# Kernel optimization log

Hardware: AMD Instinct MI355X
Metric: run time of the kernel (lower is better)

Reference implementation:

```python
import jax, jax.numpy as jnp
import numpy as np

N = 128
MAX_LEN = 1024
L = 1024
BATCH = 32


def _legs_transition(n):
    # HiPPO-LegS A, B matrices (float64 numpy, matches torch module's transition())
    q = np.arange(n, dtype=np.float64)
    col, row = np.meshgrid(q, q)
    r = 2 * q + 1
    M = -(np.where(row >= col, r, 0) - np.diag(q))
    T = np.sqrt(np.diag(2 * q + 1))
    A = T @ M @ np.linalg.inv(T)
    B = np.diag(T)
    return A, B


def _stacked_bilinear(n, max_length):
    # Bilinear discretization per timestep t: (I - A/(2t))^{-1} (I + A/(2t)), (I - A/(2t))^{-1} B/t
    A, B = _legs_transition(n)
    t = np.arange(1, max_length + 1, dtype=np.float64)[:, None, None]  # (L,1,1)
    I = np.eye(n)
    At = A[None] / t                                   # (L,N,N)
    lhs = I - At / 2
    A_st = np.linalg.solve(lhs, I + At / 2)            # (L,N,N)
    Bt = (B[None, :] / t[:, 0, 0][:, None])[..., None]  # (L,N,1)
    B_st = np.linalg.solve(lhs, Bt)[..., 0]            # (L,N)
    return A_st.astype(np.float32), B_st.astype(np.float32)


def setup_inputs() -> dict:
    key = jax.random.key(0)
    inputs = jax.random.normal(key, (L, BATCH), dtype=jnp.float32)
    A_st, B_st = _stacked_bilinear(N, MAX_LEN)
    return {
        "inputs": inputs,
        "A_stacked": jnp.asarray(A_st),
        "B_stacked": jnp.asarray(B_st),
    }


def reference(inputs, A_stacked, B_stacked):
    # inputs: (L, B); A_stacked: (L, N, N); B_stacked: (L, N)
    Lc = inputs.shape[0]
    u = inputs[..., None] * B_stacked[:Lc, None, :]  # (L, B, N)

    def step(s, Au):
        A_t, u_t = Au                                 # (N,N), (B,N)
        s = jnp.einsum("ij,bj->bi", A_t, s) + u_t
        return s, s

    s0 = jnp.zeros_like(u[0])
    _, xs = jax.lax.scan(step, s0, (A_stacked[:Lc], u))
    return xs  # (L, B, N)
```

## Files before the change

kernel.cpp:

```cpp
#include <hip/hip_runtime.h>


#define LDK 136
#define PKF 11264

using f16 = _Float16;
typedef __attribute__((ext_vector_type(8))) f16 f16x8;
typedef __attribute__((ext_vector_type(4))) f16 f16x4;
typedef __attribute__((ext_vector_type(4))) float f32x4;

__device__ __forceinline__ f32x4 mfma3(f16x8 ah, f16x8 al, f16x8 bh, f16x8 bl,
                                       f32x4 c) {
  c = __builtin_amdgcn_mfma_f32_16x16x32_f16(ah, bh, c, 0, 0, 0);
  c = __builtin_amdgcn_mfma_f32_16x16x32_f16(ah, bl, c, 0, 0, 0);
  c = __builtin_amdgcn_mfma_f32_16x16x32_f16(al, bh, c, 0, 0, 0);
  return c;
}

__device__ __forceinline__ void split8(const float* v, f16x8& h, f16x8& l) {
#pragma unroll
  for (int j = 0; j < 8; ++j) {
    const float x = v[j];
    const f16 hh = (f16)x;
    h[j] = hh;
    l[j] = (f16)(x - (float)hh);
  }
}

__device__ __forceinline__ int slot2mt(int h, int slot) {
  if (h == 0) return (slot & 1) ? 7 - (slot >> 1) : (slot >> 1);
  return (slot & 1) ? 5 - (slot >> 1) : 2 + (slot >> 1);
}

__device__ __forceinline__ void gload_lds16(const float* g, float* l) {
  __builtin_amdgcn_global_load_lds(
      (const __attribute__((address_space(1))) unsigned int*)g,
      (__attribute__((address_space(3))) unsigned int*)l, 16, 0, 0);
}

__device__ __forceinline__ void bar_nodrain() {
  __builtin_amdgcn_sched_barrier(0);
  asm volatile("s_waitcnt lgkmcnt(0)" ::: "memory");
  __builtin_amdgcn_s_barrier();
  __builtin_amdgcn_sched_barrier(0);
}
__device__ __forceinline__ void wait_vm0() {
  __builtin_amdgcn_sched_barrier(0);
  asm volatile("s_waitcnt vmcnt(0)" ::: "memory");
  __builtin_amdgcn_sched_barrier(0);
}

__device__ __forceinline__ int pk_src_off(int m) {
  int b, local, ccm1, sh;
  if (m < 128)      { b = 0; local = m;       ccm1 = 3;  sh = 2; }
  else if (m < 384) { b = 1; local = m - 128; ccm1 = 7;  sh = 3; }
  else if (m < 896) { b = 2; local = m - 384; ccm1 = 15; sh = 4; }
  else              { b = 3; local = m - 896; ccm1 = 15; sh = 4; }
  const int ri = local >> sh, cp = local & ccm1;
  const int c = cp ^ (ri & ccm1);
  return (b * 32 + ri) * 128 + c * 8;
}

__device__ __forceinline__ void read_pk(const f16* __restrict__ Bs, int nt,
                                        int lr, int j0, f16x8& v) {
  const int b = nt >> 1;
  const int ri = ((nt & 1) << 4) + lr;
  const int ccm1 = (b == 0) ? 3 : (b == 1) ? 7 : 15;
  const int fb = (b == 0) ? 0 : (b == 1) ? 1024 : (b == 2) ? 3072 : 7168;
  const int c = j0 ^ (ri & ccm1);
  v = *(const f16x8*)(Bs + fb + ri * ((ccm1 + 1) * 8) + c * 8);
}

template <int NT, int IT>
__device__ __forceinline__ void pk_precompute(int tid, int (&src)[IT]) {
#pragma unroll
  for (int it = 0; it < IT; ++it) {
    const int m = tid + it * NT;
    src[it] = (m < 1408) ? pk_src_off(m) : 0;
  }
}

template <int NT, int IT>
__device__ __forceinline__ void pk_stage(const f16* __restrict__ gMh,
                                         const f16* __restrict__ gMl,
                                         f16* __restrict__ dH,
                                         f16* __restrict__ dL,
                                         const int (&src)[IT], int tid) {
#pragma unroll
  for (int it = 0; it < IT; ++it) {
    const int m = tid + it * NT;
    if (m < 1408) {
      gload_lds16((const float*)(gMh + src[it]), (float*)(dH + m * 8));
      gload_lds16((const float*)(gMl + src[it]), (float*)(dL + m * 8));
    }
  }
}

__device__ __forceinline__ void compute_soff(int tid, int (&soff)[8]) {
#pragma unroll
  for (int it = 0; it < 8; ++it) {
    const int m = tid + it * 320;
    if (m < 2304) {
      const int kt = (m >= 768) + (m >= 1536) + (m >= 2048);
      const int local = m - ((kt >= 1) * 768 + (kt >= 2) * 768 + (kt >= 3) * 512);
      const int rp = local >> 3, c = local & 7;
      const int r = rp + 32 + (kt >= 2) * 32 + (kt >= 3) * 32;
      soff[it] = r * 128 + kt * 32 + ((c ^ (rp & 7)) << 2);
    } else {
      soff[it] = 0;
    }
  }
}

__device__ __forceinline__ void issue_A(const float* __restrict__ Al,
                                        float* __restrict__ Ast,
                                        const int (&soff)[8], int tid) {
#pragma unroll
  for (int it = 0; it < 8; ++it) {
    if (it < 7 || tid < 64)
      gload_lds16(Al + soff[it], Ast + (tid + it * 320) * 4);
  }
}

__device__ __forceinline__ void read_staged(const float* __restrict__ Ast,
                                            int nt, int kt, int lr, int q,
                                            f16x8& ch, f16x8& cl) {
  const int rp = nt * 16 + lr - (32 + (kt >= 2) * 32 + (kt >= 3) * 32);
  const float* pb =
      Ast + ((kt >= 1) * 3072 + (kt >= 2) * 3072 + (kt >= 3) * 2048) + rp * 32;
  float raw[8];
  *(float4*)&raw[0] = *(const float4*)(pb + (((2 * q + 0) ^ (rp & 7)) << 2));
  *(float4*)&raw[4] = *(const float4*)(pb + (((2 * q + 1) ^ (rp & 7)) << 2));
  split8(raw, ch, cl);
}

__device__ __forceinline__ void chain_step_k1a(const float* __restrict__ Acur,
                                               const float* __restrict__ Anext,
                                               const float* __restrict__ x32,
                                               const float* __restrict__ Bvl,
                                               f16* __restrict__ Ph,
                                               f16* __restrict__ Pl,
                                               const float* __restrict__ AstCur,
                                               float* __restrict__ AstNxt,
                                               const int (&soff)[8],
                                               int wv, int mt) {
  const int tid = threadIdx.x;
  const int lane = tid & 63, lr = lane & 15, q = lane >> 4;
  const bool wrow = (mt >= 8);
  const int ktA0 = wrow ? 0 : (mt >> 1);
  f16x8 ah[4], al[4];
#pragma unroll
  for (int kt = 0; kt < 4; ++kt) {
    if (kt >= ktA0) {
      const int off = (wv * 16 + lr) * LDK + kt * 32 + q * 8;
      ah[kt] = *(const f16x8*)(Ph + off);
      al[kt] = *(const f16x8*)(Pl + off);
    }
  }
  const bool need0 = wrow || mt == 0;
  const bool need1 = wrow || mt <= 1;
  float dir0[8], dir1[8];
  if (need0) {
    const float* p = Acur + lr * 128 + q * 8;
    *(float4*)&dir0[0] = *(const float4*)p;
    *(float4*)&dir0[4] = *(const float4*)(p + 4);
  }
  if (need1) {
    const float* p = Acur + (16 + lr) * 128 + q * 8;
    *(float4*)&dir1[0] = *(const float4*)p;
    *(float4*)&dir1[4] = *(const float4*)(p + 4);
  }
  float4 x4v = {0.f, 0.f, 0.f, 0.f};
  float bnv[8];
  if (wrow) {
    const int b0 = (mt - 8) * 16 + q * 4;
    x4v = *(const float4*)(x32 + b0);
#pragma unroll
    for (int nt = 0; nt < 8; ++nt) bnv[nt] = Bvl[nt * 16 + lr];
  }
  wait_vm0();
  bar_nodrain();
  if (Anext) issue_A(Anext, AstNxt, soff, tid);
  f32x4 acc[8];
#pragma unroll
  for (int nt = 0; nt < 8; ++nt) acc[nt] = (f32x4){0.f, 0.f, 0.f, 0.f};
#pragma unroll
  for (int nt = 2; nt < 8; ++nt) {
    if (wrow || nt >= mt) {
#pragma unroll
      for (int kt = 0; kt < 4; ++kt) {
        if (kt >= ktA0 && kt <= (nt >> 1)) {
          f16x8 ch, cl;
          read_staged(AstCur, nt, kt, lr, q, ch, cl);
          acc[nt] = mfma3(ah[kt], al[kt], ch, cl, acc[nt]);
        }
      }
    }
  }
  if (need0) {
    f16x8 ch, cl;
    split8(dir0, ch, cl);
    acc[0] = mfma3(ah[0], al[0], ch, cl, acc[0]);
  }
  if (need1) {
    f16x8 ch, cl;
    split8(dir1, ch, cl);
    acc[1] = mfma3(ah[0], al[0], ch, cl, acc[1]);
  }
#pragma unroll
  for (int nt = 0; nt < 8; ++nt) {
    if (!(wrow || nt >= mt)) continue;
    float v[4] = {acc[nt][0], acc[nt][1], acc[nt][2], acc[nt][3]};
    if (wrow) {
      v[0] += bnv[nt] * x4v.x; v[1] += bnv[nt] * x4v.y;
      v[2] += bnv[nt] * x4v.z; v[3] += bnv[nt] * x4v.w;
    }
#pragma unroll
    for (int r = 0; r < 4; ++r) {
      const int o = (wv * 16 + q * 4 + r) * LDK + nt * 16 + lr;
      const f16 hh = (f16)v[r];
      Ph[o] = hh;
      Pl[o] = (f16)(v[r] - (float)hh);
    }
  }
  bar_nodrain();
}

__device__ __forceinline__ void chain_copyout(const f16* __restrict__ Ph,
                                              const f16* __restrict__ Pl, int h,
                                              f16* __restrict__ oMh,
                                              f16* __restrict__ oMl,
                                              float* __restrict__ oW) {
  const int tid = threadIdx.x;
  for (int t = tid; t < 1024; t += 320) {
    const int i = t >> 3;
    const int slot = (t >> 1) & 3;
    const int half = t & 1;
    const int mtg = slot2mt(h, slot);
    const int y0 = mtg * 16 + half * 8;
    if ((y0 >> 5) > (i >> 5)) continue;
    f16x8 hv, lv;
#pragma unroll
    for (int e = 0; e < 8; ++e) {
      hv[e] = Ph[(slot * 16 + half * 8 + e) * LDK + i];
      lv[e] = Pl[(slot * 16 + half * 8 + e) * LDK + i];
    }
    *(f16x8*)(oMh + i * 128 + y0) = hv;
    *(f16x8*)(oMl + i * 128 + y0) = lv;
  }
  for (int t = tid; t < 512; t += 320) {
    const int n = t >> 2, b4 = (t & 3) * 4;
    float4 o;
    float* po = (float*)&o;
#pragma unroll
    for (int e = 0; e < 4; ++e)
      po[e] = (float)Ph[(64 + b4 + e) * LDK + n] + (float)Pl[(64 + b4 + e) * LDK + n];
    *(float4*)(oW + n * 32 + h * 16 + b4) = o;
  }
}

__device__ __forceinline__ void state_step_h_b16(const f16* __restrict__ Bh16,
                                                 const f16* __restrict__ Bl16,
                                                 const float* __restrict__ aux0,
                                                 f16* __restrict__ Sh,
                                                 f16* __restrict__ Sl, int h) {
  const int tid = threadIdx.x;
  const int wv4 = tid >> 6;
  const bool act = (wv4 < 4);
  const int wv = wv4 & 3;
  const int lane = tid & 63, lr = lane & 15, q = lane >> 4;
  const int nts[2] = {wv, 7 - wv};
  const int ktAmax = (7 - wv) >> 1;
  f16x8 ah[4], al[4];
  f16x8 bh[2][4], bl[2][4];
  f32x4 acc[2];
  if (act) {
#pragma unroll
    for (int kt = 0; kt < 4; ++kt)
      if (kt <= ktAmax) {
        const int off = lr * LDK + kt * 32 + q * 8;
        ah[kt] = *(const f16x8*)(Sh + off);
        al[kt] = *(const f16x8*)(Sl + off);
      }
#pragma unroll
    for (int ni = 0; ni < 2; ++ni) {
      const int nt = nts[ni];
#pragma unroll
      for (int kt = 0; kt < 4; ++kt)
        if (kt <= (nt >> 1)) {
          const int o = (nt * 16 + lr) * 128 + kt * 32 + q * 8;
          bh[ni][kt] = *(const f16x8*)(Bh16 + o);
          bl[ni][kt] = *(const f16x8*)(Bl16 + o);
        }
    }
#pragma unroll
    for (int ni = 0; ni < 2; ++ni) acc[ni] = (f32x4){0.f, 0.f, 0.f, 0.f};
#pragma unroll
    for (int ni = 0; ni < 2; ++ni) {
      const int nt = nts[ni];
#pragma unroll
      for (int kt = 0; kt < 4; ++kt)
        if (kt <= (nt >> 1))
          acc[ni] = mfma3(ah[kt], al[kt], bh[ni][kt], bl[ni][kt], acc[ni]);
    }
  }
  __syncthreads();
  if (act) {
#pragma unroll
    for (int ni = 0; ni < 2; ++ni) {
      const int nt = nts[ni];
      float v[4] = {acc[ni][0], acc[ni][1], acc[ni][2], acc[ni][3]};
      const int bq = q * 4;
      const float4 w4 = *(const float4*)(aux0 + (nt * 16 + lr) * 32 + h * 16 + bq);
      v[0] += w4.x; v[1] += w4.y; v[2] += w4.z; v[3] += w4.w;
#pragma unroll
      for (int r = 0; r < 4; ++r) {
        const int o = (bq + r) * LDK + nt * 16 + lr;
        const f16 hh = (f16)v[r];
        Sh[o] = hh;
        Sl[o] = (f16)(v[r] - (float)hh);
      }
    }
  }
  __syncthreads();
}

__device__ __forceinline__ void state_step_h_stagedA(
    const float* __restrict__ Acur, const float* __restrict__ Anext,
    const float* __restrict__ x32, const float* __restrict__ Bvl,
    f16* __restrict__ Sh, f16* __restrict__ Sl, float* __restrict__ outp,
    int h, const float* __restrict__ AstCur, float* __restrict__ AstNxt,
    const int (&soff)[8]) {
  const int tid = threadIdx.x;
  const int wv4 = tid >> 6;
  const bool act = (wv4 < 4);
  const int wv = wv4 & 3;
  const int lane = tid & 63, lr = lane & 15, q = lane >> 4;
  const int ntL = wv, ntH = 7 - wv;
  f16x8 ah[4], al[4];
  float dir[8];
  float4 x4v = {0.f, 0.f, 0.f, 0.f};
  float bnL = 0.f, bnH = 0.f;
  if (act) {
    const int ktAmax = ntH >> 1;
#pragma unroll
    for (int kt = 0; kt < 4; ++kt)
      if (kt <= ktAmax) {
        const int off = lr * LDK + kt * 32 + q * 8;
        ah[kt] = *(const f16x8*)(Sh + off);
        al[kt] = *(const f16x8*)(Sl + off);
      }
    if (wv < 2) {
      const float* p = Acur + (ntL * 16 + lr) * 128 + q * 8;
      *(float4*)&dir[0] = *(const float4*)p;
      *(float4*)&dir[4] = *(const float4*)(p + 4);
    }
    x4v = *(const float4*)(x32 + h * 16 + q * 4);
    bnL = Bvl[ntL * 16 + lr];
    bnH = Bvl[ntH * 16 + lr];
  }
  wait_vm0();
  bar_nodrain();
  if (Anext) issue_A(Anext, AstNxt, soff, tid);
  f32x4 accL = (f32x4){0.f, 0.f, 0.f, 0.f}, accH = accL;
  if (act) {
#pragma unroll
    for (int kt = 0; kt < 4; ++kt) {
      if (kt <= (ntH >> 1)) {
        f16x8 ch, cl;
        read_staged(AstCur, ntH, kt, lr, q, ch, cl);
        accH = mfma3(ah[kt], al[kt], ch, cl, accH);
      }
    }
    if (wv >= 2) {
#pragma unroll
      for (int kt = 0; kt < 4; ++kt) {
        if (kt <= (ntL >> 1)) {
          f16x8 ch, cl;
          read_staged(AstCur, ntL, kt, lr, q, ch, cl);
          accL = mfma3(ah[kt], al[kt], ch, cl, accL);
        }
      }
    } else {
      f16x8 ch, cl;
      split8(dir, ch, cl);
      accL = mfma3(ah[0], al[0], ch, cl, accL);
    }
  }
  if (act) {
#pragma unroll
    for (int ni = 0; ni < 2; ++ni) {
      const int nt = (ni == 0) ? ntL : ntH;
      const float bn = (ni == 0) ? bnL : bnH;
      const f32x4 a = (ni == 0) ? accL : accH;
      float v[4] = {a[0], a[1], a[2], a[3]};
      const int bq = q * 4;
      v[0] += bn * x4v.x; v[1] += bn * x4v.y;
      v[2] += bn * x4v.z; v[3] += bn * x4v.w;
      if (outp) {
#pragma unroll
        for (int r = 0; r < 4; ++r)
          outp[(h * 16 + bq + r) * 128 + nt * 16 + lr] = v[r];
      }
#pragma unroll
      for (int r = 0; r < 4; ++r) {
        const int o = (bq + r) * LDK + nt * 16 + lr;
        const f16 hh = (f16)v[r];
        Sh[o] = hh;
        Sl[o] = (f16)(v[r] - (float)hh);
      }
    }
  }
  bar_nodrain();
}

__global__ __launch_bounds__(320) void k1_chunks(const float* __restrict__ A,
                                                 const float* __restrict__ x,
                                                 const float* __restrict__ Bv,
                                                 f16* __restrict__ Mh,
                                                 f16* __restrict__ Ml,
                                                 float* __restrict__ Wf) {
  __shared__ f16 Ph[80 * LDK], Pl[80 * LDK];
  __shared__ float Ast[2][9216];
  const int tid = threadIdx.x;
  const int c = blockIdx.x >> 1, h = blockIdx.x & 1;
  const int l0 = 4 * c;
  int soff[8];
  compute_soff(tid, soff);
  issue_A(A + (size_t)(l0 + 1) * 16384, Ast[1], soff, tid);
  const float* A0 = A + (size_t)l0 * 16384;
  for (int t = tid; t < 2048; t += 320) {
    const int k = t >> 4, u = t & 15;
    const int slot = u >> 2, fo = (u & 3) * 4;
    const int mtg = slot2mt(h, slot);
    const int y = mtg * 16 + fo;
    float vv[4];
    if ((y >> 5) <= (k >> 5)) {
      const float4 v = *(const float4*)(A0 + k * 128 + y);
      vv[0] = v.x; vv[1] = v.y; vv[2] = v.z; vv[3] = v.w;
    } else {
      vv[0] = vv[1] = vv[2] = vv[3] = 0.f;
    }
#pragma unroll
    for (int e = 0; e < 4; ++e) {
      const f16 hh = (f16)vv[e];
      Ph[(slot * 16 + fo + e) * LDK + k] = hh;
      Pl[(slot * 16 + fo + e) * LDK + k] = (f16)(vv[e] - (float)hh);
    }
  }
  for (int t = tid; t < 512; t += 320) {
    const int b = t >> 5, n4 = (t & 31) * 4;
    const float xb = x[l0 * 32 + h * 16 + b];
#pragma unroll
    for (int e = 0; e < 4; ++e) {
      const float u = xb * Bv[l0 * 128 + n4 + e];
      const f16 hh = (f16)u;
      Ph[(64 + b) * LDK + n4 + e] = hh;
      Pl[(64 + b) * LDK + n4 + e] = (f16)(u - (float)hh);
    }
  }
  bar_nodrain();
  const int wv = tid >> 6;
  const int mt = (wv == 4) ? (8 + h) : slot2mt(h, wv);
  chain_step_k1a(A + (size_t)(l0 + 1) * 16384, A + (size_t)(l0 + 2) * 16384,
                 x + (l0 + 1) * 32, Bv + (l0 + 1) * 128, Ph, Pl,
                 Ast[1], Ast[0], soff, wv, mt);
  chain_step_k1a(A + (size_t)(l0 + 2) * 16384, A + (size_t)(l0 + 3) * 16384,
                 x + (l0 + 2) * 32, Bv + (l0 + 2) * 128, Ph, Pl,
                 Ast[0], Ast[1], soff, wv, mt);
  chain_step_k1a(A + (size_t)(l0 + 3) * 16384, nullptr,
                 x + (l0 + 3) * 32, Bv + (l0 + 3) * 128, Ph, Pl,
                 Ast[1], Ast[0], soff, wv, mt);
  chain_copyout(Ph, Pl, h, Mh + (size_t)c * 16384, Ml + (size_t)c * 16384,
                Wf + (size_t)c * 4096);
}

__global__ __launch_bounds__(192) void mscan_s(const f16* __restrict__ MhA,
                                               const f16* __restrict__ MlA,
                                               const float* __restrict__ WA,
                                               f16* __restrict__ MhB,
                                               f16* __restrict__ MlB,
                                               float* __restrict__ WB) {
  __shared__ f16 Ph[48 * LDK], Pl[48 * LDK];
  __shared__ f16 BstH[2][PKF], BstL[2][PKF];
  const int bid = blockIdx.x;
  const int g = bid & 15, unit = bid >> 4;
  const int h = unit >> 1, half = unit & 1;
  const int tid = threadIdx.x;
  const int wv = tid >> 6;
  const int lane = tid & 63, lr = lane & 15, q = lane >> 4;
  const bool isW = (half == 0 && wv == 2);
  const bool isM = (wv < 2);
  const int mt = isW ? (8 + h) : (isM ? slot2mt(h, half * 2 + wv) : 0);
  const int lw = wv * 16;
  const int ktA0 = isW ? 0 : (mt >> 1);
  const size_t n0 = (size_t)(16 * g);

  int src[8];
  pk_precompute<192, 8>(tid, src);
  pk_stage<192, 8>(MhA + (n0 + 1) * 16384, MlA + (n0 + 1) * 16384,
                   BstH[1], BstL[1], src, tid);
  if (isM) {
    const f16* pMh = MhA + n0 * 16384;
    const f16* pMl = MlA + n0 * 16384;
#pragma unroll
    for (int it = 0; it < 4; ++it) {
      const int t = lane + it * 64;
      const int k = t >> 1, hk = t & 1;
      const int y0 = mt * 16 + hk * 8;
      f16x8 hv, lv;
      if ((y0 >> 5) <= (k >> 5)) {
        hv = *(const f16x8*)(pMh + k * 128 + y0);
        lv = *(const f16x8*)(pMl + k * 128 + y0);
      } else {
#pragma unroll
        for (int e = 0; e < 8; ++e) { hv[e] = (f16)0.f; lv[e] = (f16)0.f; }
      }
#pragma unroll
      for (int e = 0; e < 8; ++e) {
        Ph[(lw + hk * 8 + e) * LDK + k] = hv[e];
        Pl[(lw + hk * 8 + e) * LDK + k] = lv[e];
      }
    }
  } else if (isW) {
    const float* pW = WA + n0 * 4096;
#pragma unroll
    for (int it = 0; it < 8; ++it) {
      const int t = lane + it * 64;
      const int n = t >> 2, b4 = (t & 3) * 4;
      const float4 w4 = *(const float4*)(pW + n * 32 + h * 16 + b4);
      const float vv[4] = {w4.x, w4.y, w4.z, w4.w};
#pragma unroll
      for (int r = 0; r < 4; ++r) {
        const f16 hh = (f16)vv[r];
        Ph[(lw + b4 + r) * LDK + n] = hh;
        Pl[(lw + b4 + r) * LDK + n] = (f16)(vv[r] - (float)hh);
      }
    }
  }
  __syncthreads();

#pragma unroll 1
  for (int j = 1; j <= 15; ++j) {
    const size_t nd = n0 + j;
    const int cur = j & 1;
    if (j < 15)
      pk_stage<192, 8>(MhA + (nd + 1) * 16384, MlA + (nd + 1) * 16384,
                       BstH[cur ^ 1], BstL[cur ^ 1], src, tid);
    float4 w4s[8];
    if (isW) {
      const float* Wn = WA + nd * 4096;
#pragma unroll
      for (int nt = 0; nt < 8; ++nt)
        w4s[nt] = *(const float4*)(Wn + (nt * 16 + lr) * 32 + h * 16 + q * 4);
    }
    f16x8 ah[4], al[4];
    if (isM || isW) {
#pragma unroll
      for (int kt = 0; kt < 4; ++kt)
        if (kt >= ktA0) {
          const int off = (lw + lr) * LDK + kt * 32 + q * 8;
          ah[kt] = *(const f16x8*)(Ph + off);
          al[kt] = *(const f16x8*)(Pl + off);
        }
    }
    f32x4 acc[8];
#pragma unroll
    for (int nt = 0; nt < 8; ++nt) acc[nt] = (f32x4){0.f, 0.f, 0.f, 0.f};
    if (isM || isW) {
      const int ntF = isW ? 0 : mt;
#pragma unroll
      for (int nt = 0; nt < 8; ++nt) {
        if (nt >= ntF) {
#pragma unroll
          for (int kt = 0; kt < 4; ++kt) {
            if (kt >= ktA0 && kt <= (nt >> 1)) {
              f16x8 bh, bl;
              const int j0 = kt * 4 + q;
              read_pk(BstH[cur], nt, lr, j0, bh);
              read_pk(BstL[cur], nt, lr, j0, bl);
              acc[nt] = mfma3(ah[kt], al[kt], bh, bl, acc[nt]);
            }
          }
        }
      }
    }
    if (isM) {
      f16* oMh = MhB + nd * 16384;
      f16* oMl = MlB + nd * 16384;
      if (mt & 1) {
        const int k = (mt - 1) * 16 + lr;
        const f16x4 z = {(f16)0.f, (f16)0.f, (f16)0.f, (f16)0.f};
        *(f16x4*)(oMh + k * 128 + mt * 16 + q * 4) = z;
        *(f16x4*)(oMl + k * 128 + mt * 16 + q * 4) = z;
      }
#pragma unroll
      for (int nt = 0; nt < 8; ++nt) {
        if (nt < mt) continue;
        f16x4 hv4, lv4;
#pragma unroll
        for (int r = 0; r < 4; ++r) {
          const float v = acc[nt][r];
          const f16 hh = (f16)v;
          const f16 ll = (f16)(v - (float)hh);
          hv4[r] = hh;
          lv4[r] = ll;
          Ph[(lw + q * 4 + r) * LDK + nt * 16 + lr] = hh;
          Pl[(lw + q * 4 + r) * LDK + nt * 16 + lr] = ll;
        }
        const int k = nt * 16 + lr;
        *(f16x4*)(oMh + k * 128 + mt * 16 + q * 4) = hv4;
        *(f16x4*)(oMl + k * 128 + mt * 16 + q * 4) = lv4;
      }
    } else if (isW) {
      float* oW = WB + nd * 4096;
#pragma unroll
      for (int nt = 0; nt < 8; ++nt) {
        float v[4];
#pragma unroll
        for (int r = 0; r < 4; ++r) v[r] = acc[nt][r];
        v[0] += w4s[nt].x; v[1] += w4s[nt].y; v[2] += w4s[nt].z; v[3] += w4s[nt].w;
#pragma unroll
        for (int r = 0; r < 4; ++r) {
          const f16 hh = (f16)v[r];
          Ph[(lw + q * 4 + r) * LDK + nt * 16 + lr] = hh;
          Pl[(lw + q * 4 + r) * LDK + nt * 16 + lr] = (f16)(v[r] - (float)hh);
        }
        const float4 o = {v[0], v[1], v[2], v[3]};
        *(float4*)(oW + (nt * 16 + lr) * 32 + h * 16 + q * 4) = o;
      }
    }
    __syncthreads();
  }
}

__global__ __launch_bounds__(256) void gscan(const f16* __restrict__ MhB,
                                             const f16* __restrict__ MlB,
                                             const float* __restrict__ WB,
                                             float* __restrict__ Ef) {
  __shared__ f16 Sh[16 * LDK], Sl[16 * LDK];
  __shared__ f16 GstH[2][PKF], GstL[2][PKF];
  const int g = blockIdx.x & 15, h = blockIdx.x >> 4;
  const int tid = threadIdx.x;
  int src[6];
  pk_precompute<256, 6>(tid, src);
  for (int t = tid; t < 16 * LDK; t += 256) { Sh[t] = (f16)0.f; Sl[t] = (f16)0.f; }
  if (g > 0)
    pk_stage<256, 6>(MhB + (size_t)15 * 16384, MlB + (size_t)15 * 16384,
                     GstH[0], GstL[0], src, tid);
  __syncthreads();
  const int wv = (tid >> 6) & 3;
  const int lane = tid & 63, lr = lane & 15, q = lane >> 4;
  const int nts[2] = {wv, 7 - wv};
  const int ktAmax = (7 - wv) >> 1;
#pragma unroll 1
  for (int t = 0; t < g; ++t) {
    const size_t nd = (size_t)(16 * t + 15);
    const int cur = t & 1;
    if (t + 1 < g) {
      const size_t nn = (size_t)(16 * (t + 1) + 15);
      pk_stage<256, 6>(MhB + nn * 16384, MlB + nn * 16384,
                       GstH[cur ^ 1], GstL[cur ^ 1], src, tid);
    }
    const float* aux0 = WB + nd * 4096;
    float4 w4s[2];
#pragma unroll
    for (int ni = 0; ni < 2; ++ni)
      w4s[ni] = *(const float4*)(aux0 + (nts[ni] * 16 + lr) * 32 + h * 16 + q * 4);
    f16x8 ah[4], al[4];
#pragma unroll
    for (int kt = 0; kt < 4; ++kt)
      if (kt <= ktAmax) {
        const int off = lr * LDK + kt * 32 + q * 8;
        ah[kt] = *(const f16x8*)(Sh + off);
        al[kt] = *(const f16x8*)(Sl + off);
      }
    f32x4 acc[2];
#pragma unroll
    for (int ni = 0; ni < 2; ++ni) acc[ni] = (f32x4){0.f, 0.f, 0.f, 0.f};
#pragma unroll
    for (int ni = 0; ni < 2; ++ni) {
      const int nt = nts[ni];
#pragma unroll
      for (int kt = 0; kt < 4; ++kt)
        if (kt <= (nt >> 1)) {
          f16x8 bh, bl;
          const int j0 = kt * 4 + q;
          read_pk(GstH[cur], nt, lr, j0, bh);
          read_pk(GstL[cur], nt, lr, j0, bl);
          acc[ni] = mfma3(ah[kt], al[kt], bh, bl, acc[ni]);
        }
    }
    __syncthreads();
#pragma unroll
    for (int ni = 0; ni < 2; ++ni) {
      const int nt = nts[ni];
      float v[4] = {acc[ni][0], acc[ni][1], acc[ni][2], acc[ni][3]};
      v[0] += w4s[ni].x; v[1] += w4s[ni].y; v[2] += w4s[ni].z; v[3] += w4s[ni].w;
#pragma unroll
      for (int r = 0; r < 4; ++r) {
        const int o = (q * 4 + r) * LDK + nt * 16 + lr;
        const f16 hh = (f16)v[r];
        Sh[o] = hh;
        Sl[o] = (f16)(v[r] - (float)hh);
      }
    }
    __syncthreads();
  }
  for (int t = tid; t < 2048; t += 256) {
    const int row = t & 15, n = t >> 4;
    Ef[(size_t)g * 4096 + n * 32 + h * 16 + row] =
        (float)Sh[row * LDK + n] + (float)Sl[row * LDK + n];
  }
}

__global__ __launch_bounds__(320) void k3h(const float* __restrict__ A,
                                           const float* __restrict__ x,
                                           const float* __restrict__ Bv,
                                           const f16* __restrict__ MhA,
                                           const f16* __restrict__ MlA,
                                           const float* __restrict__ WA,
                                           const f16* __restrict__ MhB,
                                           const f16* __restrict__ MlB,
                                           const float* __restrict__ WB,
                                           const float* __restrict__ Ef,
                                           float* __restrict__ out) {
  __shared__ f16 Sh[16 * LDK], Sl[16 * LDK];
  __shared__ float Ast[2][9216];
  const int tid = threadIdx.x;
  const int c = blockIdx.x >> 1, h = blockIdx.x & 1;
  const int g = c >> 4, j = c & 15;
  int soff[8];
  compute_soff(tid, soff);
  issue_A(A + (size_t)(4 * c) * 16384, Ast[0], soff, tid);
  const float* Ew = Ef + (size_t)g * 4096;
  for (int tt = tid; tt < 2048; tt += 320) {
    const int row = tt & 15, n = tt >> 4;
    const float v = Ew[n * 32 + h * 16 + row];
    const f16 hh = (f16)v;
    Sh[row * LDK + n] = hh;
    Sl[row * LDK + n] = (f16)(v - (float)hh);
  }
  bar_nodrain();
  if (j > 0) {
    const int nd = c - 1, jp = j - 1;
    const bool inA = (jp == 0);
    const f16* mh = (inA ? MhA : MhB) + (size_t)nd * 16384;
    const f16* ml = (inA ? MlA : MlB) + (size_t)nd * 16384;
    const float* w = (inA ? WA : WB) + (size_t)nd * 4096;
    state_step_h_b16(mh, ml, w, Sh, Sl, h);
  }
#pragma unroll 1
  for (int t4 = 0; t4 < 4; ++t4) {
    const int l = 4 * c + t4;
    const float* Anext = (t4 < 3) ? A + (size_t)(l + 1) * 16384 : nullptr;
    state_step_h_stagedA(A + (size_t)l * 16384, Anext, x + l * 32,
                         Bv + l * 128, Sh, Sl, out + (size_t)l * 4096, h,
                         Ast[t4 & 1], (float*)Ast[(t4 + 1) & 1], soff);
  }
}

extern "C" void kernel_launch(void* const* d_in, const int* in_sizes, int n_in,
                              void* d_out, int out_size, void* d_ws, size_t ws_size,
                              hipStream_t stream) {
  const float* x  = (const float*)d_in[0];
  const float* A  = (const float*)d_in[1];
  const float* Bv = (const float*)d_in[2];
  float* out = (float*)d_out;

  f16* MhA = (f16*)d_ws;
  f16* MlA = MhA + 256 * 16384;
  float* WA = (float*)(MlA + 256 * 16384);
  f16* MhB = (f16*)(WA + 256 * 4096);
  f16* MlB = MhB + 256 * 16384;
  float* WB = (float*)(MlB + 256 * 16384);
  float* Ef = WB + 256 * 4096;

  k1_chunks<<<512, 320, 0, stream>>>(A, x, Bv, MhA, MlA, WA);
  mscan_s<<<64, 192, 0, stream>>>(MhA, MlA, WA, MhB, MlB, WB);
  gscan<<<32, 256, 0, stream>>>(MhB, MlB, WB, Ef);
  k3h<<<512, 320, 0, stream>>>(A, x, Bv, MhA, MlA, WA, MhB, MlB, WB, Ef, out);
}
```

Baseline: 250.8 us.

## Prefetch next-step A direct rows and W offsets one step ahead across kernels

After: 238.6 us. 4.9% less time.

```diff
diff --git a/kernel.cpp b/kernel.cpp
--- a/kernel.cpp
+++ b/kernel.cpp
@@ -134,8 +134,7 @@
   split8(raw, ch, cl);
 }
 
-__device__ __forceinline__ void chain_step_k1a(const float* __restrict__ Acur,
-                                               const float* __restrict__ Anext,
+__device__ __forceinline__ void chain_step_k1a(const float* __restrict__ Anext,
                                                const float* __restrict__ x32,
                                                const float* __restrict__ Bvl,
                                                f16* __restrict__ Ph,
@@ -143,11 +142,15 @@
                                                const float* __restrict__ AstCur,
                                                float* __restrict__ AstNxt,
                                                const int (&soff)[8],
-                                               int wv, int mt) {
+                                               int wv, int mt,
+                                               float (&dir0)[8], float (&dir1)[8],
+                                               const float* __restrict__ AdirNext) {
   const int tid = threadIdx.x;
   const int lane = tid & 63, lr = lane & 15, q = lane >> 4;
   const bool wrow = (mt >= 8);
   const int ktA0 = wrow ? 0 : (mt >> 1);
+  const bool need0 = wrow || mt == 0;
+  const bool need1 = wrow || mt <= 1;
   f16x8 ah[4], al[4];
 #pragma unroll
   for (int kt = 0; kt < 4; ++kt) {
@@ -157,18 +160,20 @@
       al[kt] = *(const f16x8*)(Pl + off);
     }
   }
-  const bool need0 = wrow || mt == 0;
-  const bool need1 = wrow || mt <= 1;
-  float dir0[8], dir1[8];
-  if (need0) {
-    const float* p = Acur + lr * 128 + q * 8;
-    *(float4*)&dir0[0] = *(const float4*)p;
-    *(float4*)&dir0[4] = *(const float4*)(p + 4);
-  }
-  if (need1) {
-    const float* p = Acur + (16 + lr) * 128 + q * 8;
-    *(float4*)&dir1[0] = *(const float4*)p;
-    *(float4*)&dir1[4] = *(const float4*)(p + 4);
+  wait_vm0();
+  bar_nodrain();
+  float dirN0[8], dirN1[8];
+  if (AdirNext) {
+    if (need0) {
+      const float* p = AdirNext + lr * 128 + q * 8;
+      *(float4*)&dirN0[0] = *(const float4*)p;
+      *(float4*)&dirN0[4] = *(const float4*)(p + 4);
+    }
+    if (need1) {
+      const float* p = AdirNext + (16 + lr) * 128 + q * 8;
+      *(float4*)&dirN1[0] = *(const float4*)p;
+      *(float4*)&dirN1[4] = *(const float4*)(p + 4);
+    }
   }
   float4 x4v = {0.f, 0.f, 0.f, 0.f};
   float bnv[8];
@@ -178,8 +183,6 @@
 #pragma unroll
     for (int nt = 0; nt < 8; ++nt) bnv[nt] = Bvl[nt * 16 + lr];
   }
-  wait_vm0();
-  bar_nodrain();
   if (Anext) issue_A(Anext, AstNxt, soff, tid);
   f32x4 acc[8];
 #pragma unroll
@@ -221,6 +224,16 @@
       const f16 hh = (f16)v[r];
       Ph[o] = hh;
       Pl[o] = (f16)(v[r] - (float)hh);
+    }
+  }
+  if (AdirNext) {
+    if (need0) {
+#pragma unroll
+      for (int e = 0; e < 8; ++e) dir0[e] = dirN0[e];
+    }
+    if (need1) {
+#pragma unroll
+      for (int e = 0; e < 8; ++e) dir1[e] = dirN1[e];
     }
   }
   bar_nodrain();
@@ -326,11 +339,11 @@
 }
 
 __device__ __forceinline__ void state_step_h_stagedA(
-    const float* __restrict__ Acur, const float* __restrict__ Anext,
-    const float* __restrict__ x32, const float* __restrict__ Bvl,
-    f16* __restrict__ Sh, f16* __restrict__ Sl, float* __restrict__ outp,
-    int h, const float* __restrict__ AstCur, float* __restrict__ AstNxt,
-    const int (&soff)[8]) {
+    const float* __restrict__ Anext, const float* __restrict__ x32,
+    const float* __restrict__ Bvl, f16* __restrict__ Sh, f16* __restrict__ Sl,
+    float* __restrict__ outp, int h, const float* __restrict__ AstCur,
+    float* __restrict__ AstNxt, const int (&soff)[8], float (&dir)[8],
+    const float* __restrict__ AdirNext) {
   const int tid = threadIdx.x;
   const int wv4 = tid >> 6;
   const bool act = (wv4 < 4);
@@ -338,9 +351,6 @@
   const int lane = tid & 63, lr = lane & 15, q = lane >> 4;
   const int ntL = wv, ntH = 7 - wv;
   f16x8 ah[4], al[4];
-  float dir[8];
-  float4 x4v = {0.f, 0.f, 0.f, 0.f};
-  float bnL = 0.f, bnH = 0.f;
   if (act) {
     const int ktAmax = ntH >> 1;
 #pragma unroll
@@ -350,17 +360,22 @@
         ah[kt] = *(const f16x8*)(Sh + off);
         al[kt] = *(const f16x8*)(Sl + off);
       }
-    if (wv < 2) {
-      const float* p = Acur + (ntL * 16 + lr) * 128 + q * 8;
-      *(float4*)&dir[0] = *(const float4*)p;
-      *(float4*)&dir[4] = *(const float4*)(p + 4);
-    }
+  }
+  wait_vm0();
+  bar_nodrain();
+  float dirN[8];
+  if (AdirNext && act && wv < 2) {
+    const float* p = AdirNext + (ntL * 16 + lr) * 128 + q * 8;
+    *(float4*)&dirN[0] = *(const float4*)p;
+    *(float4*)&dirN[4] = *(const float4*)(p + 4);
+  }
+  float4 x4v = {0.f, 0.f, 0.f, 0.f};
+  float bnL = 0.f, bnH = 0.f;
+  if (act) {
     x4v = *(const float4*)(x32 + h * 16 + q * 4);
     bnL = Bvl[ntL * 16 + lr];
     bnH = Bvl[ntH * 16 + lr];
   }
-  wait_vm0();
-  bar_nodrain();
   if (Anext) issue_A(Anext, AstNxt, soff, tid);
   f32x4 accL = (f32x4){0.f, 0.f, 0.f, 0.f}, accH = accL;
   if (act) {
@@ -410,6 +425,10 @@
         Sl[o] = (f16)(v[r] - (float)hh);
       }
     }
+  }
+  if (AdirNext && act && wv < 2) {
+#pragma unroll
+    for (int e = 0; e < 8; ++e) dir[e] = dirN[e];
   }
   bar_nodrain();
 }
@@ -425,8 +444,28 @@
   const int tid = threadIdx.x;
   const int c = blockIdx.x >> 1, h = blockIdx.x & 1;
   const int l0 = 4 * c;
+  const int lane = tid & 63, lr = lane & 15, q = lane >> 4;
+  const int wv = tid >> 6;
+  const int mt = (wv == 4) ? (8 + h) : slot2mt(h, wv);
+  const bool wrow = (mt >= 8);
+  const bool need0 = wrow || mt == 0;
+  const bool need1 = wrow || mt <= 1;
   int soff[8];
   compute_soff(tid, soff);
+  float dir0[8], dir1[8];
+  {
+    const float* A1 = A + (size_t)(l0 + 1) * 16384;
+    if (need0) {
+      const float* p = A1 + lr * 128 + q * 8;
+      *(float4*)&dir0[0] = *(const float4*)p;
+      *(float4*)&dir0[4] = *(const float4*)(p + 4);
+    }
+    if (need1) {
+      const float* p = A1 + (16 + lr) * 128 + q * 8;
+      *(float4*)&dir1[0] = *(const float4*)p;
+      *(float4*)&dir1[4] = *(const float4*)(p + 4);
+    }
+  }
   issue_A(A + (size_t)(l0 + 1) * 16384, Ast[1], soff, tid);
   const float* A0 = A + (size_t)l0 * 16384;
   for (int t = tid; t < 2048; t += 320) {
@@ -460,17 +499,14 @@
     }
   }
   bar_nodrain();
-  const int wv = tid >> 6;
-  const int mt = (wv == 4) ? (8 + h) : slot2mt(h, wv);
-  chain_step_k1a(A + (size_t)(l0 + 1) * 16384, A + (size_t)(l0 + 2) * 16384,
-                 x + (l0 + 1) * 32, Bv + (l0 + 1) * 128, Ph, Pl,
-                 Ast[1], Ast[0], soff, wv, mt);
-  chain_step_k1a(A + (size_t)(l0 + 2) * 16384, A + (size_t)(l0 + 3) * 16384,
-                 x + (l0 + 2) * 32, Bv + (l0 + 2) * 128, Ph, Pl,
-                 Ast[0], Ast[1], soff, wv, mt);
-  chain_step_k1a(A + (size_t)(l0 + 3) * 16384, nullptr,
-                 x + (l0 + 3) * 32, Bv + (l0 + 3) * 128, Ph, Pl,
-                 Ast[1], Ast[0], soff, wv, mt);
+  chain_step_k1a(A + (size_t)(l0 + 2) * 16384, x + (l0 + 1) * 32,
+                 Bv + (l0 + 1) * 128, Ph, Pl, Ast[1], Ast[0], soff, wv, mt,
+                 dir0, dir1, A + (size_t)(l0 + 2) * 16384);
+  chain_step_k1a(A + (size_t)(l0 + 3) * 16384, x + (l0 + 2) * 32,
+                 Bv + (l0 + 2) * 128, Ph, Pl, Ast[0], Ast[1], soff, wv, mt,
+                 dir0, dir1, A + (size_t)(l0 + 3) * 16384);
+  chain_step_k1a(nullptr, x + (l0 + 3) * 32, Bv + (l0 + 3) * 128, Ph, Pl,
+                 Ast[1], Ast[0], soff, wv, mt, dir0, dir1, nullptr);
   chain_copyout(Ph, Pl, h, Mh + (size_t)c * 16384, Ml + (size_t)c * 16384,
                 Wf + (size_t)c * 4096);
 }
@@ -544,16 +580,16 @@
   for (int j = 1; j <= 15; ++j) {
     const size_t nd = n0 + j;
     const int cur = j & 1;
+    float4 w4s[8];
+    if (isW) {
+      const float* Wn = WA + nd * 4096;
+#pragma unroll
+      for (int nt = 0; nt < 8; ++nt)
+        w4s[nt] = *(const float4*)(Wn + (nt * 16 + lr) * 32 + h * 16 + q * 4);
+    }
     if (j < 15)
       pk_stage<192, 8>(MhA + (nd + 1) * 16384, MlA + (nd + 1) * 16384,
                        BstH[cur ^ 1], BstL[cur ^ 1], src, tid);
-    float4 w4s[8];
-    if (isW) {
-      const float* Wn = WA + nd * 4096;
-#pragma unroll
-      for (int nt = 0; nt < 8; ++nt)
-        w4s[nt] = *(const float4*)(Wn + (nt * 16 + lr) * 32 + h * 16 + q * 4);
-    }
     f16x8 ah[4], al[4];
     if (isM || isW) {
 #pragma unroll
@@ -594,40 +630,50 @@
         *(f16x4*)(oMh + k * 128 + mt * 16 + q * 4) = z;
         *(f16x4*)(oMl + k * 128 + mt * 16 + q * 4) = z;
       }
+      f16x4 hv4s[8], lv4s[8];
 #pragma unroll
       for (int nt = 0; nt < 8; ++nt) {
         if (nt < mt) continue;
-        f16x4 hv4, lv4;
 #pragma unroll
         for (int r = 0; r < 4; ++r) {
           const float v = acc[nt][r];
           const f16 hh = (f16)v;
-          const f16 ll = (f16)(v - (float)hh);
-          hv4[r] = hh;
-          lv4[r] = ll;
-          Ph[(lw + q * 4 + r) * LDK + nt * 16 + lr] = hh;
-          Pl[(lw + q * 4 + r) * LDK + nt * 16 + lr] = ll;
+          hv4s[nt][r] = hh;
+          lv4s[nt][r] = (f16)(v - (float)hh);
         }
         const int k = nt * 16 + lr;
-        *(f16x4*)(oMh + k * 128 + mt * 16 + q * 4) = hv4;
-        *(f16x4*)(oMl + k * 128 + mt * 16 + q * 4) = lv4;
+        *(f16x4*)(oMh + k * 128 + mt * 16 + q * 4) = hv4s[nt];
+        *(f16x4*)(oMl + k * 128 + mt * 16 + q * 4) = lv4s[nt];
+      }
+#pragma unroll
+      for (int nt = 0; nt < 8; ++nt) {
+        if (nt < mt) continue;
+#pragma unroll
+        for (int r = 0; r < 4; ++r) {
+          Ph[(lw + q * 4 + r) * LDK + nt * 16 + lr] = hv4s[nt][r];
+          Pl[(lw + q * 4 + r) * LDK + nt * 16 + lr] = lv4s[nt][r];
+        }
       }
     } else if (isW) {
       float* oW = WB + nd * 4096;
+      float vs[8][4];
 #pragma unroll
       for (int nt = 0; nt < 8; ++nt) {
-        float v[4];
-#pragma unroll
-        for (int r = 0; r < 4; ++r) v[r] = acc[nt][r];
-        v[0] += w4s[nt].x; v[1] += w4s[nt].y; v[2] += w4s[nt].z; v[3] += w4s[nt].w;
+#pragma unroll
+        for (int r = 0; r < 4; ++r) vs[nt][r] = acc[nt][r];
+        vs[nt][0] += w4s[nt].x; vs[nt][1] += w4s[nt].y;
+        vs[nt][2] += w4s[nt].z; vs[nt][3] += w4s[nt].w;
+        const float4 o = {vs[nt][0], vs[nt][1], vs[nt][2], vs[nt][3]};
+        *(float4*)(oW + (nt * 16 + lr) * 32 + h * 16 + q * 4) = o;
+      }
+#pragma unroll
+      for (int nt = 0; nt < 8; ++nt) {
 #pragma unroll
         for (int r = 0; r < 4; ++r) {
-          const f16 hh = (f16)v[r];
+          const f16 hh = (f16)vs[nt][r];
           Ph[(lw + q * 4 + r) * LDK + nt * 16 + lr] = hh;
-          Pl[(lw + q * 4 + r) * LDK + nt * 16 + lr] = (f16)(v[r] - (float)hh);
+          Pl[(lw + q * 4 + r) * LDK + nt * 16 + lr] = (f16)(vs[nt][r] - (float)hh);
         }
-        const float4 o = {v[0], v[1], v[2], v[3]};
-        *(float4*)(oW + (nt * 16 + lr) * 32 + h * 16 + q * 4) = o;
       }
     }
     __syncthreads();
@@ -644,29 +690,34 @@
   const int tid = threadIdx.x;
   int src[6];
   pk_precompute<256, 6>(tid, src);
-  for (int t = tid; t < 16 * LDK; t += 256) { Sh[t] = (f16)0.f; Sl[t] = (f16)0.f; }
-  if (g > 0)
-    pk_stage<256, 6>(MhB + (size_t)15 * 16384, MlB + (size_t)15 * 16384,
-                     GstH[0], GstL[0], src, tid);
-  __syncthreads();
   const int wv = (tid >> 6) & 3;
   const int lane = tid & 63, lr = lane & 15, q = lane >> 4;
   const int nts[2] = {wv, 7 - wv};
   const int ktAmax = (7 - wv) >> 1;
+  for (int t = tid; t < 16 * LDK; t += 256) { Sh[t] = (f16)0.f; Sl[t] = (f16)0.f; }
+  float4 w4c[2];
+  if (g > 0) {
+    const float* a0 = WB + (size_t)15 * 4096;
+    w4c[0] = *(const float4*)(a0 + (nts[0] * 16 + lr) * 32 + h * 16 + q * 4);
+    w4c[1] = *(const float4*)(a0 + (nts[1] * 16 + lr) * 32 + h * 16 + q * 4);
+    pk_stage<256, 6>(MhB + (size_t)15 * 16384, MlB + (size_t)15 * 16384,
+                     GstH[0], GstL[0], src, tid);
+  }
+  bar_nodrain();
 #pragma unroll 1
   for (int t = 0; t < g; ++t) {
-    const size_t nd = (size_t)(16 * t + 15);
     const int cur = t & 1;
+    wait_vm0();
+    bar_nodrain();
+    float4 w4n[2];
     if (t + 1 < g) {
       const size_t nn = (size_t)(16 * (t + 1) + 15);
+      const float* an = WB + nn * 4096;
+      w4n[0] = *(const float4*)(an + (nts[0] * 16 + lr) * 32 + h * 16 + q * 4);
+      w4n[1] = *(const float4*)(an + (nts[1] * 16 + lr) * 32 + h * 16 + q * 4);
       pk_stage<256, 6>(MhB + nn * 16384, MlB + nn * 16384,
                        GstH[cur ^ 1], GstL[cur ^ 1], src, tid);
     }
-    const float* aux0 = WB + nd * 4096;
-    float4 w4s[2];
-#pragma unroll
-    for (int ni = 0; ni < 2; ++ni)
-      w4s[ni] = *(const float4*)(aux0 + (nts[ni] * 16 + lr) * 32 + h * 16 + q * 4);
     f16x8 ah[4], al[4];
 #pragma unroll
     for (int kt = 0; kt < 4; ++kt)
@@ -691,12 +742,12 @@
           acc[ni] = mfma3(ah[kt], al[kt], bh, bl, acc[ni]);
         }
     }
-    __syncthreads();
+    bar_nodrain();
 #pragma unroll
     for (int ni = 0; ni < 2; ++ni) {
       const int nt = nts[ni];
       float v[4] = {acc[ni][0], acc[ni][1], acc[ni][2], acc[ni][3]};
-      v[0] += w4s[ni].x; v[1] += w4s[ni].y; v[2] += w4s[ni].z; v[3] += w4s[ni].w;
+      v[0] += w4c[ni].x; v[1] += w4c[ni].y; v[2] += w4c[ni].z; v[3] += w4c[ni].w;
 #pragma unroll
       for (int r = 0; r < 4; ++r) {
         const int o = (q * 4 + r) * LDK + nt * 16 + lr;
@@ -705,7 +756,8 @@
         Sl[o] = (f16)(v[r] - (float)hh);
       }
     }
-    __syncthreads();
+    if (t + 1 < g) { w4c[0] = w4n[0]; w4c[1] = w4n[1]; }
+    bar_nodrain();
   }
   for (int t = tid; t < 2048; t += 256) {
     const int row = t & 15, n = t >> 4;
@@ -730,8 +782,16 @@
   const int tid = threadIdx.x;
   const int c = blockIdx.x >> 1, h = blockIdx.x & 1;
   const int g = c >> 4, j = c & 15;
+  const int lane = tid & 63, lr = lane & 15, q = lane >> 4;
   int soff[8];
   compute_soff(tid, soff);
+  float dir[8];
+  if (tid < 128) {
+    const int ntL = tid >> 6;
+    const float* p = A + (size_t)(4 * c) * 16384 + (ntL * 16 + lr) * 128 + q * 8;
+    *(float4*)&dir[0] = *(const float4*)p;
+    *(float4*)&dir[4] = *(const float4*)(p + 4);
+  }
   issue_A(A + (size_t)(4 * c) * 16384, Ast[0], soff, tid);
   const float* Ew = Ef + (size_t)g * 4096;
   for (int tt = tid; tt < 2048; tt += 320) {
@@ -754,9 +814,9 @@
   for (int t4 = 0; t4 < 4; ++t4) {
     const int l = 4 * c + t4;
     const float* Anext = (t4 < 3) ? A + (size_t)(l + 1) * 16384 : nullptr;
-    state_step_h_stagedA(A + (size_t)l * 16384, Anext, x + l * 32,
-                         Bv + l * 128, Sh, Sl, out + (size_t)l * 4096, h,
-                         Ast[t4 & 1], (float*)Ast[(t4 + 1) & 1], soff);
+    state_step_h_stagedA(Anext, x + l * 32, Bv + l * 128, Sh, Sl,
+                         out + (size_t)l * 4096, h, Ast[t4 & 1],
+                         (float*)Ast[(t4 + 1) & 1], soff, dir, Anext);
   }
 }
 
```
